# Optimization experiments

Measured on AMD Instinct MI355X. Metric: run time of the kernel, lower is better.

Reference implementation:

```python
import jax, jax.numpy as jnp
import numpy as np

ALPHA = 0.2  # LeakyReLU negative slope used by GAT attention


def _seg_softmax(scores, rows, n):
    # numerically stable softmax of per-edge scores grouped by destination row
    m = jax.ops.segment_max(scores, rows, num_segments=n)
    ex = jnp.exp(scores - m[rows])
    s = jax.ops.segment_sum(ex, rows, num_segments=n)
    return ex / s[rows]


def setup_inputs() -> dict:
    key = jax.random.key(0)
    ks = jax.random.split(key, 10)
    VOCAB, U, N, DEG = 200000, 50000, 20000, 16
    DIN, DOUT, H, ETYPES, EDIM = 64, 64, 4, 32, 64
    node_features = jax.random.normal(ks[0], (VOCAB, DIN), jnp.float32)
    W = jax.random.normal(ks[1], (H, DIN, DOUT), jnp.float32) * np.float32(np.sqrt(2.0 / (DIN + DOUT)))
    a_pos = jax.random.normal(ks[2], (H, 2 * DOUT), jnp.float32) * 0.1
    a_neg = jax.random.normal(ks[3], (H, 2 * DOUT), jnp.float32) * 0.1
    edge_embedding = jax.random.normal(ks[4], (ETYPES, EDIM), jnp.float32)
    edge_transform = jax.random.normal(ks[5], (EDIM, DOUT), jnp.float32) * np.float32(np.sqrt(2.0 / (EDIM + DOUT)))
    unique_nodes = jax.random.randint(ks[6], (U,), 0, VOCAB)
    row_unique = jax.random.randint(ks[7], (N,), 0, U)  # index of each output row's own node in the unique list
    # pos adjacency with self edges appended (adj_pos2 in the source)
    pos_row = jnp.concatenate([jnp.repeat(jnp.arange(N), DEG), jnp.arange(N)])
    pos_col = jnp.concatenate([jax.random.randint(ks[8], (N * DEG,), 0, U), row_unique])
    neg_row = jnp.repeat(jnp.arange(N), DEG)
    neg_col = jax.random.randint(ks[9], (N * DEG,), 0, U)
    return {
        "node_features": node_features, "W": W, "a_pos": a_pos, "a_neg": a_neg,
        "edge_embedding": edge_embedding, "edge_transform": edge_transform,
        "unique_nodes": unique_nodes, "row_unique": row_unique,
        "pos_row": pos_row, "pos_col": pos_col, "neg_row": neg_row, "neg_col": neg_col,
        "n_rows": N,
    }


def reference(node_features, W, a_pos, a_neg, edge_embedding, edge_transform,
              unique_nodes, row_unique, pos_row, pos_col, neg_row, neg_col, n_rows):
    embed = node_features[unique_nodes]                 # [U, Din] gather of unique node embeddings
    Wh = jnp.einsum('ud,hdo->huo', embed, W)            # [H, U, Dout]
    Dout = W.shape[-1]
    rows_all = jnp.concatenate([pos_row, neg_row])
    cols_all = jnp.concatenate([pos_col, neg_col])

    def head(Wh_h, ap, an):
        # per-node score halves (GAT trick: a^T[h_i || h_j] = a_dst.h_i + a_src.h_j)
        dst_p = (Wh_h @ ap[:Dout])[row_unique]          # [N]
        src_p = Wh_h @ ap[Dout:]                        # [U]
        dst_n = (Wh_h @ an[:Dout])[row_unique]
        src_n = Wh_h @ an[Dout:]
        e_pos = jax.nn.leaky_relu(dst_p[pos_row] + src_p[pos_col], ALPHA)
        e_neg = jax.nn.leaky_relu(dst_n[neg_row] + src_n[neg_col], ALPHA)
        att = _seg_softmax(jnp.concatenate([e_pos, e_neg]), rows_all, n_rows)  # joint softmax over pos+neg edges
        return jax.ops.segment_sum(att[:, None] * Wh_h[cols_all], rows_all, num_segments=n_rows)

    outs = jax.vmap(head)(Wh, a_pos, a_neg)             # [H, N, Dout]
    h_hidden = jax.nn.relu(jnp.transpose(outs, (1, 0, 2)).reshape(outs.shape[1], -1))  # concat heads -> ReLU
    edge_out = edge_embedding @ edge_transform          # edge-type projection
    return (h_hidden, edge_out)
```

## Files before the change

kernel.cpp:

```cpp
#include <hip/hip_runtime.h>
#include <hip/hip_bf16.h>
#include <hip/hip_fp16.h>
#include <math.h>

#define LRELU_ALPHA 0.2f

typedef __attribute__((ext_vector_type(8))) short bf16x8;
typedef __attribute__((ext_vector_type(4))) float f32x4;
typedef _Float16 f16x8 __attribute__((ext_vector_type(8)));

__device__ __forceinline__ unsigned short f2bf(float f) {
    union { float f; unsigned u; } v; v.f = f;
    unsigned r = v.u + 0x7fffu + ((v.u >> 16) & 1u);
    return (unsigned short)(r >> 16);
}
__device__ __forceinline__ unsigned short f2h(float f) {
    union { __half h; unsigned short s; } c; c.h = __float2half_rn(f); return c.s;
}
__device__ __forceinline__ unsigned cvtpk(float lo, float hi) {
    unsigned r;
    asm("v_cvt_pk_bf16_f32 %0, %1, %2" : "=v"(r) : "v"(lo), "v"(hi));
    return r;
}
__device__ __forceinline__ __half2 u2h2(unsigned u) {
    union { unsigned u; __half2 h; } x; x.u = u; return x.h;
}
__device__ __forceinline__ unsigned h22u(__half2 h) {
    union { __half2 h; unsigned u; } x; x.h = h; return x.u;
}
__device__ __forceinline__ float2 upk(unsigned u) {
    return __half22float2(u2h2(u));
}

__global__ void prep_kernel(const float* __restrict__ W,
                            const float* __restrict__ a_pos, const float* __restrict__ a_neg,
                            const float* __restrict__ ee, const float* __restrict__ et,
                            unsigned short* __restrict__ Wt, unsigned short* __restrict__ avB,
                            float* __restrict__ edge_out, int H, int ET) {
    const int HE = H * 4096, AV = H * 256;
    int t = blockIdx.x * blockDim.x + threadIdx.x;
    if (t < HE) {
        int k = t & 63, n = (t >> 6) & 63, h = t >> 12;
        Wt[((size_t)h * 64 + n) * 64 + k] = f2h(W[(size_t)h * 4096 + k * 64 + n]);
    } else if (t < HE + AV) {
        int s = t - HE;
        int k = s & 63, q = (s >> 6) & 3, h = s >> 8;
        const float* a  = (q < 2 ? a_pos : a_neg) + (size_t)h * 128 + (q & 1) * 64;
        const float* wr = W + (size_t)h * 4096 + k * 64;
        float v = 0.f;
#pragma unroll
        for (int o = 0; o < 64; o += 4) {
            const float4 wv = *(const float4*)(wr + o);
            const float4 av = *(const float4*)(a + o);
            v = fmaf(wv.x, av.x, fmaf(wv.y, av.y, fmaf(wv.z, av.z, fmaf(wv.w, av.w, v))));
        }
        avB[((size_t)h * 4 + q) * 64 + k] = f2bf(v);
    } else {
        int s = t - HE - AV;
        if (s < ET * 64) {
            int e = s >> 6, o = s & 63;
            float acc = 0.f;
#pragma unroll
            for (int k = 0; k < 64; ++k)
                acc = fmaf(ee[e * 64 + k], et[k * 64 + o], acc);
            edge_out[s] = acc;
        }
    }
}

__global__ __launch_bounds__(256) void score_cvt_kernel(
    const float* __restrict__ nf, const unsigned short* __restrict__ avB,
    const int* __restrict__ un, unsigned short* __restrict__ embed16,
    unsigned* __restrict__ scd, unsigned* __restrict__ scs, int U)
{
    const int wave = threadIdx.x >> 6;
    const int lane = threadIdx.x & 63;
    const int grp  = lane >> 4;
    const int r    = lane & 15;
    const long u0  = (long)blockIdx.x * 64 + wave * 16;
    if (u0 >= U) return;
    const long u  = u0 + r;
    const long ur = (u < U) ? u : (long)(U - 1);

    const float* erow = nf + (size_t)un[ur] * 64 + grp * 8;
    const float4 e0 = *(const float4*)(erow);
    const float4 e1 = *(const float4*)(erow + 4);
    const float4 e2 = *(const float4*)(erow + 32);
    const float4 e3 = *(const float4*)(erow + 36);

    union { unsigned d[4]; bf16x8 v; } A0, A1;
    A0.d[0] = cvtpk(e0.x, e0.y); A0.d[1] = cvtpk(e0.z, e0.w);
    A0.d[2] = cvtpk(e1.x, e1.y); A0.d[3] = cvtpk(e1.z, e1.w);
    A1.d[0] = cvtpk(e2.x, e2.y); A1.d[1] = cvtpk(e2.z, e2.w);
    A1.d[2] = cvtpk(e3.x, e3.y); A1.d[3] = cvtpk(e3.z, e3.w);

    if (u < U) {
        union { __half2 h2[4]; uint4 v; } F0, F1;
        F0.h2[0] = __floats2half2_rn(e0.x, e0.y); F0.h2[1] = __floats2half2_rn(e0.z, e0.w);
        F0.h2[2] = __floats2half2_rn(e1.x, e1.y); F0.h2[3] = __floats2half2_rn(e1.z, e1.w);
        F1.h2[0] = __floats2half2_rn(e2.x, e2.y); F1.h2[1] = __floats2half2_rn(e2.z, e2.w);
        F1.h2[2] = __floats2half2_rn(e3.x, e3.y); F1.h2[3] = __floats2half2_rn(e3.z, e3.w);
        *(uint4*)(embed16 + (size_t)u * 64 + grp * 8)      = F0.v;
        *(uint4*)(embed16 + (size_t)u * 64 + 32 + grp * 8) = F1.v;
    }

    f32x4 acc = (f32x4)(0.f);
    const unsigned short* wp = avB + (size_t)r * 64 + grp * 8;
    bf16x8 b0 = *(const bf16x8*)wp;
    bf16x8 b1 = *(const bf16x8*)(wp + 32);
    acc = __builtin_amdgcn_mfma_f32_16x16x32_bf16(b0, A0.v, acc, 0, 0, 0);
    acc = __builtin_amdgcn_mfma_f32_16x16x32_bf16(b1, A1.v, acc, 0, 0, 0);

    if (u < U) {
        scd[(size_t)u * 4 + grp] = h22u(__floats2half2_rn(acc[0], acc[2]));
        scs[(size_t)u * 4 + grp] = h22u(__floats2half2_rn(acc[1], acc[3]));
    }
}

__global__ __launch_bounds__(512) void aggemm_kernel(
    const int* __restrict__ pos_col, const int* __restrict__ neg_col,
    const unsigned short* __restrict__ embed16,
    const unsigned* __restrict__ scd, const unsigned* __restrict__ scs,
    const unsigned short* __restrict__ Wt,
    float* __restrict__ out, int N, int U)
{
    constexpr int DP = 16, NE = 33, NEP = 36;
    __shared__ int   s_col[8][2][NEP];
    __shared__ uint4 s_att[8][2][NEP];
    __shared__ __align__(16) unsigned short s_agg[16][256];

    const int wave = threadIdx.x >> 6;
    const int lane = threadIdx.x & 63;
    const int iA = blockIdx.x * 16 + wave * 2;
    const int iB = iA + 1;

    int colA = 0, colB = 0;
    if (lane < DP)       { colA = pos_col[(size_t)iA * DP + lane];
                           colB = pos_col[(size_t)iB * DP + lane]; }
    else if (lane == DP) { colA = pos_col[(size_t)N * DP + iA];
                           colB = pos_col[(size_t)N * DP + iB]; }
    else if (lane < NE)  { colA = neg_col[(size_t)iA * 16 + (lane - DP - 1)];
                           colB = neg_col[(size_t)iB * 16 + (lane - DP - 1)]; }

    const uint4 svA = *(const uint4*)(scs + (size_t)(unsigned)colA * 4);
    const uint4 svB = *(const uint4*)(scs + (size_t)(unsigned)colB * 4);
    const int uA = __shfl(colA, DP, 64), uB = __shfl(colB, DP, 64);
    const uint4 dvA = *(const uint4*)(scd + (size_t)(unsigned)uA * 4);
    const uint4 dvB = *(const uint4*)(scd + (size_t)(unsigned)uB * 4);

    const bool isp = (lane <= DP);
    float2 sA_0 = upk(svA.x), sA_1 = upk(svA.y), sA_2 = upk(svA.z), sA_3 = upk(svA.w);
    float2 sB_0 = upk(svB.x), sB_1 = upk(svB.y), sB_2 = upk(svB.z), sB_3 = upk(svB.w);
    float2 dA_0 = upk(dvA.x), dA_1 = upk(dvA.y), dA_2 = upk(dvA.z), dA_3 = upk(dvA.w);
    float2 dB_0 = upk(dvB.x), dB_1 = upk(dvB.y), dB_2 = upk(dvB.z), dB_3 = upk(dvB.w);
    float a_s0 = isp ? dA_0.x + sA_0.x : dA_0.y + sA_0.y;
    float a_s1 = isp ? dA_1.x + sA_1.x : dA_1.y + sA_1.y;
    float a_s2 = isp ? dA_2.x + sA_2.x : dA_2.y + sA_2.y;
    float a_s3 = isp ? dA_3.x + sA_3.x : dA_3.y + sA_3.y;
    float b_s0 = isp ? dB_0.x + sB_0.x : dB_0.y + sB_0.y;
    float b_s1 = isp ? dB_1.x + sB_1.x : dB_1.y + sB_1.y;
    float b_s2 = isp ? dB_2.x + sB_2.x : dB_2.y + sB_2.y;
    float b_s3 = isp ? dB_3.x + sB_3.x : dB_3.y + sB_3.y;
    a_s0 = (a_s0 > 0.f) ? a_s0 : LRELU_ALPHA * a_s0;
    a_s1 = (a_s1 > 0.f) ? a_s1 : LRELU_ALPHA * a_s1;
    a_s2 = (a_s2 > 0.f) ? a_s2 : LRELU_ALPHA * a_s2;
    a_s3 = (a_s3 > 0.f) ? a_s3 : LRELU_ALPHA * a_s3;
    b_s0 = (b_s0 > 0.f) ? b_s0 : LRELU_ALPHA * b_s0;
    b_s1 = (b_s1 > 0.f) ? b_s1 : LRELU_ALPHA * b_s1;
    b_s2 = (b_s2 > 0.f) ? b_s2 : LRELU_ALPHA * b_s2;
    b_s3 = (b_s3 > 0.f) ? b_s3 : LRELU_ALPHA * b_s3;

    const bool act = (lane < NE);
    float ax0 = act ? __expf(a_s0) : 0.f, ax1 = act ? __expf(a_s1) : 0.f;
    float ax2 = act ? __expf(a_s2) : 0.f, ax3 = act ? __expf(a_s3) : 0.f;
    float bx0 = act ? __expf(b_s0) : 0.f, bx1 = act ? __expf(b_s1) : 0.f;
    float bx2 = act ? __expf(b_s2) : 0.f, bx3 = act ? __expf(b_s3) : 0.f;
    float aS0 = ax0, aS1 = ax1, aS2 = ax2, aS3 = ax3;
    float bS0 = bx0, bS1 = bx1, bS2 = bx2, bS3 = bx3;
#pragma unroll
    for (int off = 32; off; off >>= 1) {
        aS0 += __shfl_xor(aS0, off, 64); aS1 += __shfl_xor(aS1, off, 64);
        aS2 += __shfl_xor(aS2, off, 64); aS3 += __shfl_xor(aS3, off, 64);
        bS0 += __shfl_xor(bS0, off, 64); bS1 += __shfl_xor(bS1, off, 64);
        bS2 += __shfl_xor(bS2, off, 64); bS3 += __shfl_xor(bS3, off, 64);
    }
    if (lane < NEP) {
        uint4 tA, tB;
        tA.x = h22u(__float2half2_rn(__fdividef(ax0, aS0)));
        tA.y = h22u(__float2half2_rn(__fdividef(ax1, aS1)));
        tA.z = h22u(__float2half2_rn(__fdividef(ax2, aS2)));
        tA.w = h22u(__float2half2_rn(__fdividef(ax3, aS3)));
        tB.x = h22u(__float2half2_rn(__fdividef(bx0, bS0)));
        tB.y = h22u(__float2half2_rn(__fdividef(bx1, bS1)));
        tB.z = h22u(__float2half2_rn(__fdividef(bx2, bS2)));
        tB.w = h22u(__float2half2_rn(__fdividef(bx3, bS3)));
        s_col[wave][0][lane] = colA;  s_att[wave][0][lane] = tA;
        s_col[wave][1][lane] = colB;  s_att[wave][1][lane] = tB;
    }

    const int sub = lane >> 4;
    const int c   = lane & 15;
    const char* eb = (const char*)embed16 + (c << 3);
    __half2 accA[4][2], accB[4][2];
#pragma unroll
    for (int h = 0; h < 4; ++h)
#pragma unroll
        for (int d = 0; d < 2; ++d) {
            accA[h][d] = __float2half2_rn(0.f);
            accB[h][d] = __float2half2_rn(0.f);
        }
#pragma unroll
    for (int t = 0; t < 9; ++t) {
        const int   e  = 4 * t + sub;
        const int   cA = s_col[wave][0][e];
        const int   cB = s_col[wave][1][e];
        const uint2 vA = *(const uint2*)(eb + ((size_t)(unsigned)cA << 7));
        const uint2 vB = *(const uint2*)(eb + ((size_t)(unsigned)cB << 7));
        const uint4 tA = s_att[wave][0][e];
        const uint4 tB = s_att[wave][1][e];
        const __half2 vA0 = u2h2(vA.x), vA1 = u2h2(vA.y);
        const __half2 vB0 = u2h2(vB.x), vB1 = u2h2(vB.y);
        accA[0][0] = __hfma2(u2h2(tA.x), vA0, accA[0][0]);
        accA[0][1] = __hfma2(u2h2(tA.x), vA1, accA[0][1]);
        accA[1][0] = __hfma2(u2h2(tA.y), vA0, accA[1][0]);
        accA[1][1] = __hfma2(u2h2(tA.y), vA1, accA[1][1]);
        accA[2][0] = __hfma2(u2h2(tA.z), vA0, accA[2][0]);
        accA[2][1] = __hfma2(u2h2(tA.z), vA1, accA[2][1]);
        accA[3][0] = __hfma2(u2h2(tA.w), vA0, accA[3][0]);
        accA[3][1] = __hfma2(u2h2(tA.w), vA1, accA[3][1]);
        accB[0][0] = __hfma2(u2h2(tB.x), vB0, accB[0][0]);
        accB[0][1] = __hfma2(u2h2(tB.x), vB1, accB[0][1]);
        accB[1][0] = __hfma2(u2h2(tB.y), vB0, accB[1][0]);
        accB[1][1] = __hfma2(u2h2(tB.y), vB1, accB[1][1]);
        accB[2][0] = __hfma2(u2h2(tB.z), vB0, accB[2][0]);
        accB[2][1] = __hfma2(u2h2(tB.z), vB1, accB[2][1]);
        accB[3][0] = __hfma2(u2h2(tB.w), vB0, accB[3][0]);
        accB[3][1] = __hfma2(u2h2(tB.w), vB1, accB[3][1]);
    }
#pragma unroll
    for (int h = 0; h < 4; ++h)
#pragma unroll
        for (int d = 0; d < 2; ++d) {
            unsigned ua = h22u(accA[h][d]);
            ua = h22u(__hadd2(u2h2(ua), u2h2((unsigned)__shfl_xor((int)ua, 16, 64))));
            ua = h22u(__hadd2(u2h2(ua), u2h2((unsigned)__shfl_xor((int)ua, 32, 64))));
            accA[h][d] = u2h2(ua);
            unsigned ub = h22u(accB[h][d]);
            ub = h22u(__hadd2(u2h2(ub), u2h2((unsigned)__shfl_xor((int)ub, 16, 64))));
            ub = h22u(__hadd2(u2h2(ub), u2h2((unsigned)__shfl_xor((int)ub, 32, 64))));
            accB[h][d] = u2h2(ub);
        }
    if (sub == 0) {
#pragma unroll
        for (int h = 0; h < 4; ++h) {
            uint2 wA, wB;
            wA.x = h22u(accA[h][0]); wA.y = h22u(accA[h][1]);
            wB.x = h22u(accB[h][0]); wB.y = h22u(accB[h][1]);
            *(uint2*)((char*)&s_agg[wave * 2][h * 64] + c * 8)     = wA;
            *(uint2*)((char*)&s_agg[wave * 2 + 1][h * 64] + c * 8) = wB;
        }
    }
    __syncthreads();

    if (wave < 4) {
        const int h   = wave;
        const int grp = lane >> 4;
        const int r   = lane & 15;
        const f16x8 a0 = *(const f16x8*)((const char*)&s_agg[r][h * 64] + grp * 16);
        const f16x8 a1 = *(const f16x8*)((const char*)&s_agg[r][h * 64 + 32] + grp * 16);
        f32x4 acc[4];
#pragma unroll
        for (int nt = 0; nt < 4; ++nt) {
            acc[nt] = (f32x4)(0.f);
            const unsigned short* wp = Wt + (((size_t)h * 64 + nt * 16 + r) * 64 + grp * 8);
            const f16x8 b0 = *(const f16x8*)wp;
            const f16x8 b1 = *(const f16x8*)(wp + 32);
            acc[nt] = __builtin_amdgcn_mfma_f32_16x16x32_f16(b0, a0, acc[nt], 0, 0, 0);
            acc[nt] = __builtin_amdgcn_mfma_f32_16x16x32_f16(b1, a1, acc[nt], 0, 0, 0);
        }
        float* orow = out + ((size_t)(blockIdx.x * 16 + r) * 4 + h) * 64;
#pragma unroll
        for (int nt = 0; nt < 4; ++nt) {
            float4 o;
            o.x = fmaxf(acc[nt][0], 0.f); o.y = fmaxf(acc[nt][1], 0.f);
            o.z = fmaxf(acc[nt][2], 0.f); o.w = fmaxf(acc[nt][3], 0.f);
            *(float4*)(orow + nt * 16 + grp * 4) = o;
        }
    }
}

__global__ void embed_cvt_generic(const float* __restrict__ nf, const int* __restrict__ un,
                                  unsigned short* __restrict__ embed16, int U) {
    long t = (long)blockIdx.x * blockDim.x + threadIdx.x;
    if (t >= (long)U * 64) return;
    embed16[t] = f2h(nf[(size_t)un[t >> 6] * 64 + (t & 63)]);
}
__global__ void score_generic(const unsigned short* __restrict__ embed16,
                              const unsigned short* __restrict__ avB,
                              unsigned* __restrict__ scd, unsigned* __restrict__ scs,
                              int U, int H) {
    long t = (long)blockIdx.x * blockDim.x + threadIdx.x;
    if (t >= (long)U * H) return;
    const long u = t / H; const int h = (int)(t % H);
    float s[4];
    for (int q = 0; q < 4; ++q) {
        float acc = 0.f;
        for (int k = 0; k < 64; ++k) {
            union { unsigned short s; __half h; } w; w.s = embed16[u * 64 + k];
            union { unsigned uu; float f; } b;
            b.uu = ((unsigned)avB[((size_t)h * 4 + q) * 64 + k]) << 16;
            acc = fmaf(__half2float(w.h), b.f, acc);
        }
        s[q] = acc;
    }
    scd[u * H + h] = h22u(__floats2half2_rn(s[0], s[2]));
    scs[u * H + h] = h22u(__floats2half2_rn(s[1], s[3]));
}
__global__ __launch_bounds__(256) void agg_generic(
    const int* __restrict__ pos_col, const int* __restrict__ neg_col,
    const unsigned short* __restrict__ embed16,
    const unsigned* __restrict__ scd, const unsigned* __restrict__ scs,
    unsigned short* __restrict__ aggb, int N, int U, int DEGP, int DEGN, int H)
{
    const int wave = threadIdx.x >> 6;
    const int lane = threadIdx.x & 63;
    const long j = (long)blockIdx.x * 4 + wave;
    const int i = (int)(j % N);
    const int h = (int)(j / N);
    if (h >= H) return;
    const int NE = DEGP + 1 + DEGN;

    int col = 0;
    if (lane < DEGP)       col = pos_col[(size_t)i * DEGP + lane];
    else if (lane == DEGP) col = pos_col[(size_t)N * DEGP + i];
    else if (lane < NE)    col = neg_col[(size_t)i * DEGN + (lane - DEGP - 1)];
    const float2 ss = upk(scs[(size_t)col * H + h]);
    const int u0s = __shfl(col, DEGP, 64);
    const float2 sd = upk(scd[(size_t)u0s * H + h]);
    float score = -INFINITY;
    if (lane < NE) {
        const float raw = (lane <= DEGP) ? sd.x + ss.x : sd.y + ss.y;
        score = (raw > 0.f) ? raw : LRELU_ALPHA * raw;
    }
    float m = score;
#pragma unroll
    for (int off = 32; off; off >>= 1) m = fmaxf(m, __shfl_xor(m, off, 64));
    const float ex = (lane < NE) ? __expf(score - m) : 0.f;
    float S = ex;
#pragma unroll
    for (int off = 32; off; off >>= 1) S += __shfl_xor(S, off, 64);
    const float att = __fdividef(ex, S);

    float acc = 0.f;
    for (int e = 0; e < NE; ++e) {
        const int   ce = __shfl(col, e, 64);
        const float ae = __shfl(att, e, 64);
        union { unsigned short s; __half h; } w;
        w.s = embed16[(size_t)(unsigned)ce * 64 + lane];
        acc = fmaf(ae, __half2float(w.h), acc);
    }
    aggb[((size_t)i * H + h) * 64 + lane] = f2h(acc);
}
__global__ __launch_bounds__(256) void out_gemm_generic(
    const unsigned short* __restrict__ aggb, const unsigned short* __restrict__ Wt,
    float* __restrict__ out, int N, int H)
{
    const int wave = threadIdx.x >> 6;
    const int lane = threadIdx.x & 63;
    const int grp  = lane >> 4;
    const int r    = lane & 15;
    const long j = (long)blockIdx.x * 4 + wave;
    const int  h = (int)(j % H);
    const long i0 = (j / H) * 16;
    if (i0 >= N) return;
    const long i  = i0 + r;
    const long ir = (i < N) ? i : (long)(N - 1);

    const unsigned short* arow = aggb + ((size_t)ir * H + h) * 64 + grp * 8;
    const f16x8 a0 = *(const f16x8*)arow;
    const f16x8 a1 = *(const f16x8*)(arow + 32);
    f32x4 acc[4];
#pragma unroll
    for (int nt = 0; nt < 4; ++nt) {
        acc[nt] = (f32x4)(0.f);
        const unsigned short* wp = Wt + (((size_t)h * 64 + nt * 16 + r) * 64 + grp * 8);
        const f16x8 b0 = *(const f16x8*)wp;
        const f16x8 b1 = *(const f16x8*)(wp + 32);
        acc[nt] = __builtin_amdgcn_mfma_f32_16x16x32_f16(b0, a0, acc[nt], 0, 0, 0);
        acc[nt] = __builtin_amdgcn_mfma_f32_16x16x32_f16(b1, a1, acc[nt], 0, 0, 0);
    }
    if (i < N) {
        float* orow = out + ((size_t)i * H + h) * 64;
#pragma unroll
        for (int nt = 0; nt < 4; ++nt) {
            float4 o;
            o.x = fmaxf(acc[nt][0], 0.f); o.y = fmaxf(acc[nt][1], 0.f);
            o.z = fmaxf(acc[nt][2], 0.f); o.w = fmaxf(acc[nt][3], 0.f);
            *(float4*)(orow + nt * 16 + grp * 4) = o;
        }
    }
}

extern "C" void kernel_launch(void* const* d_in, const int* in_sizes, int n_in,
                              void* d_out, int out_size, void* d_ws, size_t ws_size,
                              hipStream_t stream) {
    const float* nf     = (const float*)d_in[0];
    const float* W      = (const float*)d_in[1];
    const float* a_pos  = (const float*)d_in[2];
    const float* a_neg  = (const float*)d_in[3];
    const float* ee     = (const float*)d_in[4];
    const float* et     = (const float*)d_in[5];
    const int* unique_nodes = (const int*)d_in[6];
    const int* pos_col  = (const int*)d_in[9];
    const int* neg_col  = (const int*)d_in[11];

    const int U    = in_sizes[6];
    const int N    = in_sizes[7];
    const int Epos = in_sizes[8];
    const int Eneg = in_sizes[10];
    const int H    = in_sizes[1] / (64 * 64);
    const int DEGN = Eneg / N;
    const int DEGP = Epos / N - 1;
    const int ET   = in_sizes[4] / 64;

    char* ws = (char*)d_ws;
    auto alloc = [&](size_t bytes) { char* p = ws; ws += (bytes + 255) & ~(size_t)255; return p; };
    unsigned short* embed16 = (unsigned short*)alloc((size_t)U * 64 * 2);
    unsigned*       scd     = (unsigned*)alloc((size_t)U * H * 4);
    unsigned*       scs     = (unsigned*)alloc((size_t)U * H * 4);
    unsigned short* aggb    = (unsigned short*)alloc((size_t)N * H * 64 * 2);
    unsigned short* Wt      = (unsigned short*)alloc((size_t)H * 4096 * 2);
    unsigned short* avB     = (unsigned short*)alloc((size_t)H * 256 * 2);
    float* out = (float*)d_out;

    const int PT = H * 4096 + H * 256 + ET * 64;
    prep_kernel<<<(PT + 255) / 256, 256, 0, stream>>>(W, a_pos, a_neg, ee, et, Wt, avB,
                                                      out + (size_t)N * H * 64, H, ET);

    if (H == 4 && DEGP == 16 && DEGN == 16 && (N % 16) == 0) {
        score_cvt_kernel<<<(U + 63) / 64, 256, 0, stream>>>(nf, avB, unique_nodes,
                                                            embed16, scd, scs, U);
        aggemm_kernel<<<N / 16, 512, 0, stream>>>(pos_col, neg_col, embed16,
                                                  scd, scs, Wt, out, N, U);
    } else {
        embed_cvt_generic<<<(int)(((long)U * 64 + 255) / 256), 256, 0, stream>>>(
            nf, unique_nodes, embed16, U);
        score_generic<<<(int)(((long)U * H + 255) / 256), 256, 0, stream>>>(
            embed16, avB, scd, scs, U, H);
        agg_generic<<<(int)(((long)N * H + 3) / 4), 256, 0, stream>>>(
            pos_col, neg_col, embed16, scd, scs, aggb, N, U, DEGP, DEGN, H);
        const long tiles = ((long)N + 15) / 16;
        out_gemm_generic<<<(int)((tiles * H + 3) / 4), 256, 0, stream>>>(aggb, Wt, out, N, H);
    }
}
```

Baseline: 45.60 us.

## Process four rows per wave in aggregation and move W transpose into score kernel

The aggregation kernel now handles 32 rows per block (four per wave instead of two), so all eight waves run the MFMA output GEMM rather than only four. The Wt transpose/convert moves out of prep_kernel into extra blocks of score_cvt_kernel, which shrinks the prep kernel. The aim is more memory-level parallelism per wave and fuller use of the waves in the GEMM phase. In exchange, register pressure and shared memory per block rise, and the block count halves, which can reduce occupancy.

```diff
diff --git a/kernel.cpp b/kernel.cpp
--- a/kernel.cpp
+++ b/kernel.cpp
@@ -35,16 +35,12 @@
 __global__ void prep_kernel(const float* __restrict__ W,
                             const float* __restrict__ a_pos, const float* __restrict__ a_neg,
                             const float* __restrict__ ee, const float* __restrict__ et,
-                            unsigned short* __restrict__ Wt, unsigned short* __restrict__ avB,
-                            float* __restrict__ edge_out, int H, int ET) {
-    const int HE = H * 4096, AV = H * 256;
+                            unsigned short* __restrict__ avB, float* __restrict__ edge_out,
+                            int H, int ET) {
+    const int AV = H * 256;
     int t = blockIdx.x * blockDim.x + threadIdx.x;
-    if (t < HE) {
-        int k = t & 63, n = (t >> 6) & 63, h = t >> 12;
-        Wt[((size_t)h * 64 + n) * 64 + k] = f2h(W[(size_t)h * 4096 + k * 64 + n]);
-    } else if (t < HE + AV) {
-        int s = t - HE;
-        int k = s & 63, q = (s >> 6) & 3, h = s >> 8;
+    if (t < AV) {
+        int k = t & 63, q = (t >> 6) & 3, h = t >> 8;
         const float* a  = (q < 2 ? a_pos : a_neg) + (size_t)h * 128 + (q & 1) * 64;
         const float* wr = W + (size_t)h * 4096 + k * 64;
         float v = 0.f;
@@ -56,7 +52,7 @@
         }
         avB[((size_t)h * 4 + q) * 64 + k] = f2bf(v);
     } else {
-        int s = t - HE - AV;
+        int s = t - AV;
         if (s < ET * 64) {
             int e = s >> 6, o = s & 63;
             float acc = 0.f;
@@ -70,9 +66,18 @@
 
 __global__ __launch_bounds__(256) void score_cvt_kernel(
     const float* __restrict__ nf, const unsigned short* __restrict__ avB,
-    const int* __restrict__ un, unsigned short* __restrict__ embed16,
-    unsigned* __restrict__ scd, unsigned* __restrict__ scs, int U)
+    const int* __restrict__ un, const float* __restrict__ W,
+    unsigned short* __restrict__ embed16, unsigned short* __restrict__ Wt,
+    unsigned* __restrict__ scd, unsigned* __restrict__ scs, int U, int UB, int H)
 {
+    if ((int)blockIdx.x >= UB) {
+        int t = (blockIdx.x - UB) * 256 + threadIdx.x;
+        if (t < H * 4096) {
+            int k = t & 63, n = (t >> 6) & 63, h = t >> 12;
+            Wt[((size_t)h * 64 + n) * 64 + k] = f2h(W[(size_t)h * 4096 + k * 64 + n]);
+        }
+        return;
+    }
     const int wave = threadIdx.x >> 6;
     const int lane = threadIdx.x & 63;
     const int grp  = lane >> 4;
@@ -125,170 +130,146 @@
     float* __restrict__ out, int N, int U)
 {
     constexpr int DP = 16, NE = 33, NEP = 36;
-    __shared__ int   s_col[8][2][NEP];
-    __shared__ uint4 s_att[8][2][NEP];
-    __shared__ __align__(16) unsigned short s_agg[16][256];
+    __shared__ int   s_col[8][4][NEP];
+    __shared__ uint4 s_att[8][4][NEP];
+    __shared__ __align__(16) unsigned short s_agg[32][256];
 
     const int wave = threadIdx.x >> 6;
     const int lane = threadIdx.x & 63;
-    const int iA = blockIdx.x * 16 + wave * 2;
-    const int iB = iA + 1;
-
-    int colA = 0, colB = 0;
-    if (lane < DP)       { colA = pos_col[(size_t)iA * DP + lane];
-                           colB = pos_col[(size_t)iB * DP + lane]; }
-    else if (lane == DP) { colA = pos_col[(size_t)N * DP + iA];
-                           colB = pos_col[(size_t)N * DP + iB]; }
-    else if (lane < NE)  { colA = neg_col[(size_t)iA * 16 + (lane - DP - 1)];
-                           colB = neg_col[(size_t)iB * 16 + (lane - DP - 1)]; }
-
-    const uint4 svA = *(const uint4*)(scs + (size_t)(unsigned)colA * 4);
-    const uint4 svB = *(const uint4*)(scs + (size_t)(unsigned)colB * 4);
-    const int uA = __shfl(colA, DP, 64), uB = __shfl(colB, DP, 64);
-    const uint4 dvA = *(const uint4*)(scd + (size_t)(unsigned)uA * 4);
-    const uint4 dvB = *(const uint4*)(scd + (size_t)(unsigned)uB * 4);
-
-    const bool isp = (lane <= DP);
-    float2 sA_0 = upk(svA.x), sA_1 = upk(svA.y), sA_2 = upk(svA.z), sA_3 = upk(svA.w);
-    float2 sB_0 = upk(svB.x), sB_1 = upk(svB.y), sB_2 = upk(svB.z), sB_3 = upk(svB.w);
-    float2 dA_0 = upk(dvA.x), dA_1 = upk(dvA.y), dA_2 = upk(dvA.z), dA_3 = upk(dvA.w);
-    float2 dB_0 = upk(dvB.x), dB_1 = upk(dvB.y), dB_2 = upk(dvB.z), dB_3 = upk(dvB.w);
-    float a_s0 = isp ? dA_0.x + sA_0.x : dA_0.y + sA_0.y;
-    float a_s1 = isp ? dA_1.x + sA_1.x : dA_1.y + sA_1.y;
-    float a_s2 = isp ? dA_2.x + sA_2.x : dA_2.y + sA_2.y;
-    float a_s3 = isp ? dA_3.x + sA_3.x : dA_3.y + sA_3.y;
-    float b_s0 = isp ? dB_0.x + sB_0.x : dB_0.y + sB_0.y;
-    float b_s1 = isp ? dB_1.x + sB_1.x : dB_1.y + sB_1.y;
-    float b_s2 = isp ? dB_2.x + sB_2.x : dB_2.y + sB_2.y;
-    float b_s3 = isp ? dB_3.x + sB_3.x : dB_3.y + sB_3.y;
-    a_s0 = (a_s0 > 0.f) ? a_s0 : LRELU_ALPHA * a_s0;
-    a_s1 = (a_s1 > 0.f) ? a_s1 : LRELU_ALPHA * a_s1;
-    a_s2 = (a_s2 > 0.f) ? a_s2 : LRELU_ALPHA * a_s2;
-    a_s3 = (a_s3 > 0.f) ? a_s3 : LRELU_ALPHA * a_s3;
-    b_s0 = (b_s0 > 0.f) ? b_s0 : LRELU_ALPHA * b_s0;
-    b_s1 = (b_s1 > 0.f) ? b_s1 : LRELU_ALPHA * b_s1;
-    b_s2 = (b_s2 > 0.f) ? b_s2 : LRELU_ALPHA * b_s2;
-    b_s3 = (b_s3 > 0.f) ? b_s3 : LRELU_ALPHA * b_s3;
-
-    const bool act = (lane < NE);
-    float ax0 = act ? __expf(a_s0) : 0.f, ax1 = act ? __expf(a_s1) : 0.f;
-    float ax2 = act ? __expf(a_s2) : 0.f, ax3 = act ? __expf(a_s3) : 0.f;
-    float bx0 = act ? __expf(b_s0) : 0.f, bx1 = act ? __expf(b_s1) : 0.f;
-    float bx2 = act ? __expf(b_s2) : 0.f, bx3 = act ? __expf(b_s3) : 0.f;
-    float aS0 = ax0, aS1 = ax1, aS2 = ax2, aS3 = ax3;
-    float bS0 = bx0, bS1 = bx1, bS2 = bx2, bS3 = bx3;
-#pragma unroll
-    for (int off = 32; off; off >>= 1) {
-        aS0 += __shfl_xor(aS0, off, 64); aS1 += __shfl_xor(aS1, off, 64);
-        aS2 += __shfl_xor(aS2, off, 64); aS3 += __shfl_xor(aS3, off, 64);
-        bS0 += __shfl_xor(bS0, off, 64); bS1 += __shfl_xor(bS1, off, 64);
-        bS2 += __shfl_xor(bS2, off, 64); bS3 += __shfl_xor(bS3, off, 64);
-    }
-    if (lane < NEP) {
-        uint4 tA, tB;
-        tA.x = h22u(__float2half2_rn(__fdividef(ax0, aS0)));
-        tA.y = h22u(__float2half2_rn(__fdividef(ax1, aS1)));
-        tA.z = h22u(__float2half2_rn(__fdividef(ax2, aS2)));
-        tA.w = h22u(__float2half2_rn(__fdividef(ax3, aS3)));
-        tB.x = h22u(__float2half2_rn(__fdividef(bx0, bS0)));
-        tB.y = h22u(__float2half2_rn(__fdividef(bx1, bS1)));
-        tB.z = h22u(__float2half2_rn(__fdividef(bx2, bS2)));
-        tB.w = h22u(__float2half2_rn(__fdividef(bx3, bS3)));
-        s_col[wave][0][lane] = colA;  s_att[wave][0][lane] = tA;
-        s_col[wave][1][lane] = colB;  s_att[wave][1][lane] = tB;
+    const int ibase = blockIdx.x * 32 + wave * 4;
+
+#pragma unroll
+    for (int rr = 0; rr < 4; ++rr) {
+        const int i = ibase + rr;
+        int col = 0;
+        if (lane < DP)       col = pos_col[(size_t)i * DP + lane];
+        else if (lane == DP) col = pos_col[(size_t)N * DP + i];
+        else if (lane < NE)  col = neg_col[(size_t)i * 16 + (lane - DP - 1)];
+
+        const uint4 sv = *(const uint4*)(scs + (size_t)(unsigned)col * 4);
+        const int uD = __shfl(col, DP, 64);
+        const uint4 dv = *(const uint4*)(scd + (size_t)(unsigned)uD * 4);
+
+        const bool isp = (lane <= DP);
+        float2 s_0 = upk(sv.x), s_1 = upk(sv.y), s_2 = upk(sv.z), s_3 = upk(sv.w);
+        float2 d_0 = upk(dv.x), d_1 = upk(dv.y), d_2 = upk(dv.z), d_3 = upk(dv.w);
+        float c0 = isp ? d_0.x + s_0.x : d_0.y + s_0.y;
+        float c1 = isp ? d_1.x + s_1.x : d_1.y + s_1.y;
+        float c2 = isp ? d_2.x + s_2.x : d_2.y + s_2.y;
+        float c3 = isp ? d_3.x + s_3.x : d_3.y + s_3.y;
+        c0 = (c0 > 0.f) ? c0 : LRELU_ALPHA * c0;
+        c1 = (c1 > 0.f) ? c1 : LRELU_ALPHA * c1;
+        c2 = (c2 > 0.f) ? c2 : LRELU_ALPHA * c2;
+        c3 = (c3 > 0.f) ? c3 : LRELU_ALPHA * c3;
+
+        const bool act = (lane < NE);
+        float x0 = act ? __expf(c0) : 0.f, x1 = act ? __expf(c1) : 0.f;
+        float x2 = act ? __expf(c2) : 0.f, x3 = act ? __expf(c3) : 0.f;
+        float S0 = x0, S1 = x1, S2 = x2, S3 = x3;
+#pragma unroll
+        for (int off = 32; off; off >>= 1) {
+            S0 += __shfl_xor(S0, off, 64); S1 += __shfl_xor(S1, off, 64);
+            S2 += __shfl_xor(S2, off, 64); S3 += __shfl_xor(S3, off, 64);
+        }
+        if (lane < NEP) {
+            uint4 t4;
+            t4.x = h22u(__float2half2_rn(__fdividef(x0, S0)));
+            t4.y = h22u(__float2half2_rn(__fdividef(x1, S1)));
+            t4.z = h22u(__float2half2_rn(__fdividef(x2, S2)));
+            t4.w = h22u(__float2half2_rn(__fdividef(x3, S3)));
+            s_col[wave][rr][lane] = col;
+            s_att[wave][rr][lane] = t4;
+        }
     }
 
     const int sub = lane >> 4;
     const int c   = lane & 15;
     const char* eb = (const char*)embed16 + (c << 3);
-    __half2 accA[4][2], accB[4][2];
-#pragma unroll
-    for (int h = 0; h < 4; ++h)
-#pragma unroll
-        for (int d = 0; d < 2; ++d) {
-            accA[h][d] = __float2half2_rn(0.f);
-            accB[h][d] = __float2half2_rn(0.f);
-        }
+    __half2 acc[4][4][2];
+#pragma unroll
+    for (int rr = 0; rr < 4; ++rr)
+#pragma unroll
+        for (int h = 0; h < 4; ++h)
+#pragma unroll
+            for (int d = 0; d < 2; ++d)
+                acc[rr][h][d] = __float2half2_rn(0.f);
 #pragma unroll
     for (int t = 0; t < 9; ++t) {
-        const int   e  = 4 * t + sub;
-        const int   cA = s_col[wave][0][e];
-        const int   cB = s_col[wave][1][e];
-        const uint2 vA = *(const uint2*)(eb + ((size_t)(unsigned)cA << 7));
-        const uint2 vB = *(const uint2*)(eb + ((size_t)(unsigned)cB << 7));
-        const uint4 tA = s_att[wave][0][e];
-        const uint4 tB = s_att[wave][1][e];
-        const __half2 vA0 = u2h2(vA.x), vA1 = u2h2(vA.y);
-        const __half2 vB0 = u2h2(vB.x), vB1 = u2h2(vB.y);
-        accA[0][0] = __hfma2(u2h2(tA.x), vA0, accA[0][0]);
-        accA[0][1] = __hfma2(u2h2(tA.x), vA1, accA[0][1]);
-        accA[1][0] = __hfma2(u2h2(tA.y), vA0, accA[1][0]);
-        accA[1][1] = __hfma2(u2h2(tA.y), vA1, accA[1][1]);
-        accA[2][0] = __hfma2(u2h2(tA.z), vA0, accA[2][0]);
-        accA[2][1] = __hfma2(u2h2(tA.z), vA1, accA[2][1]);
-        accA[3][0] = __hfma2(u2h2(tA.w), vA0, accA[3][0]);
-        accA[3][1] = __hfma2(u2h2(tA.w), vA1, accA[3][1]);
-        accB[0][0] = __hfma2(u2h2(tB.x), vB0, accB[0][0]);
-        accB[0][1] = __hfma2(u2h2(tB.x), vB1, accB[0][1]);
-        accB[1][0] = __hfma2(u2h2(tB.y), vB0, accB[1][0]);
-        accB[1][1] = __hfma2(u2h2(tB.y), vB1, accB[1][1]);
-        accB[2][0] = __hfma2(u2h2(tB.z), vB0, accB[2][0]);
-        accB[2][1] = __hfma2(u2h2(tB.z), vB1, accB[2][1]);
-        accB[3][0] = __hfma2(u2h2(tB.w), vB0, accB[3][0]);
-        accB[3][1] = __hfma2(u2h2(tB.w), vB1, accB[3][1]);
-    }
-#pragma unroll
-    for (int h = 0; h < 4; ++h)
-#pragma unroll
-        for (int d = 0; d < 2; ++d) {
-            unsigned ua = h22u(accA[h][d]);
-            ua = h22u(__hadd2(u2h2(ua), u2h2((unsigned)__shfl_xor((int)ua, 16, 64))));
-            ua = h22u(__hadd2(u2h2(ua), u2h2((unsigned)__shfl_xor((int)ua, 32, 64))));
-            accA[h][d] = u2h2(ua);
-            unsigned ub = h22u(accB[h][d]);
-            ub = h22u(__hadd2(u2h2(ub), u2h2((unsigned)__shfl_xor((int)ub, 16, 64))));
-            ub = h22u(__hadd2(u2h2(ub), u2h2((unsigned)__shfl_xor((int)ub, 32, 64))));
-            accB[h][d] = u2h2(ub);
-        }
+        const int e = 4 * t + sub;
+#pragma unroll
+        for (int rr = 0; rr < 4; ++rr) {
+            const int   cc = s_col[wave][rr][e];
+            const uint2 vv = *(const uint2*)(eb + ((size_t)(unsigned)cc << 7));
+            const uint4 t4 = s_att[wave][rr][e];
+            const __half2 v0 = u2h2(vv.x), v1 = u2h2(vv.y);
+            acc[rr][0][0] = __hfma2(u2h2(t4.x), v0, acc[rr][0][0]);
+            acc[rr][0][1] = __hfma2(u2h2(t4.x), v1, acc[rr][0][1]);
+            acc[rr][1][0] = __hfma2(u2h2(t4.y), v0, acc[rr][1][0]);
+            acc[rr][1][1] = __hfma2(u2h2(t4.y), v1, acc[rr][1][1]);
+            acc[rr][2][0] = __hfma2(u2h2(t4.z), v0, acc[rr][2][0]);
+            acc[rr][2][1] = __hfma2(u2h2(t4.z), v1, acc[rr][2][1]);
+            acc[rr][3][0] = __hfma2(u2h2(t4.w), v0, acc[rr][3][0]);
+            acc[rr][3][1] = __hfma2(u2h2(t4.w), v1, acc[rr][3][1]);
+        }
+    }
+#pragma unroll
+    for (int rr = 0; rr < 4; ++rr)
+#pragma unroll
+        for (int h = 0; h < 4; ++h)
+#pragma unroll
+            for (int d = 0; d < 2; ++d) {
+                unsigned ua = h22u(acc[rr][h][d]);
+                ua = h22u(__hadd2(u2h2(ua), u2h2((unsigned)__shfl_xor((int)ua, 16, 64))));
+                ua = h22u(__hadd2(u2h2(ua), u2h2((unsigned)__shfl_xor((int)ua, 32, 64))));
+                acc[rr][h][d] = u2h2(ua);
+            }
     if (sub == 0) {
 #pragma unroll
-        for (int h = 0; h < 4; ++h) {
-            uint2 wA, wB;
-            wA.x = h22u(accA[h][0]); wA.y = h22u(accA[h][1]);
-            wB.x = h22u(accB[h][0]); wB.y = h22u(accB[h][1]);
-            *(uint2*)((char*)&s_agg[wave * 2][h * 64] + c * 8)     = wA;
-            *(uint2*)((char*)&s_agg[wave * 2 + 1][h * 64] + c * 8) = wB;
-        }
+        for (int rr = 0; rr < 4; ++rr)
+#pragma unroll
+            for (int h = 0; h < 4; ++h) {
+                uint2 w2;
+                w2.x = h22u(acc[rr][h][0]); w2.y = h22u(acc[rr][h][1]);
+                *(uint2*)((char*)&s_agg[wave * 4 + rr][h * 64] + c * 8) = w2;
+            }
     }
     __syncthreads();
 
-    if (wave < 4) {
-        const int h   = wave;
+    {
+        const int h   = wave & 3;
+        const int rb  = wave >> 2;
         const int grp = lane >> 4;
         const int r   = lane & 15;
-        const f16x8 a0 = *(const f16x8*)((const char*)&s_agg[r][h * 64] + grp * 16);
-        const f16x8 a1 = *(const f16x8*)((const char*)&s_agg[r][h * 64 + 32] + grp * 16);
-        f32x4 acc[4];
+        const int row = rb * 16 + r;
+        const f16x8 a0 = *(const f16x8*)((const char*)&s_agg[row][h * 64] + grp * 16);
+        const f16x8 a1 = *(const f16x8*)((const char*)&s_agg[row][h * 64 + 32] + grp * 16);
+        f32x4 acc2[4];
 #pragma unroll
         for (int nt = 0; nt < 4; ++nt) {
-            acc[nt] = (f32x4)(0.f);
+            acc2[nt] = (f32x4)(0.f);
             const unsigned short* wp = Wt + (((size_t)h * 64 + nt * 16 + r) * 64 + grp * 8);
             const f16x8 b0 = *(const f16x8*)wp;
             const f16x8 b1 = *(const f16x8*)(wp + 32);
-            acc[nt] = __builtin_amdgcn_mfma_f32_16x16x32_f16(b0, a0, acc[nt], 0, 0, 0);
-            acc[nt] = __builtin_amdgcn_mfma_f32_16x16x32_f16(b1, a1, acc[nt], 0, 0, 0);
-        }
-        float* orow = out + ((size_t)(blockIdx.x * 16 + r) * 4 + h) * 64;
+            acc2[nt] = __builtin_amdgcn_mfma_f32_16x16x32_f16(b0, a0, acc2[nt], 0, 0, 0);
+            acc2[nt] = __builtin_amdgcn_mfma_f32_16x16x32_f16(b1, a1, acc2[nt], 0, 0, 0);
+        }
+        float* orow = out + ((size_t)(blockIdx.x * 32 + row) * 4 + h) * 64;
 #pragma unroll
         for (int nt = 0; nt < 4; ++nt) {
             float4 o;
-            o.x = fmaxf(acc[nt][0], 0.f); o.y = fmaxf(acc[nt][1], 0.f);
-            o.z = fmaxf(acc[nt][2], 0.f); o.w = fmaxf(acc[nt][3], 0.f);
+            o.x = fmaxf(acc2[nt][0], 0.f); o.y = fmaxf(acc2[nt][1], 0.f);
+            o.z = fmaxf(acc2[nt][2], 0.f); o.w = fmaxf(acc2[nt][3], 0.f);
             *(float4*)(orow + nt * 16 + grp * 4) = o;
         }
     }
 }
 
+__global__ void wt_generic(const float* __restrict__ W, unsigned short* __restrict__ Wt, int HE) {
+    int t = blockIdx.x * blockDim.x + threadIdx.x;
+    if (t >= HE) return;
+    int k = t & 63, n = (t >> 6) & 63, h = t >> 12;
+    Wt[((size_t)h * 64 + n) * 64 + k] = f2h(W[(size_t)h * 4096 + k * 64 + n]);
+}
 __global__ void embed_cvt_generic(const float* __restrict__ nf, const int* __restrict__ un,
                                   unsigned short* __restrict__ embed16, int U) {
     long t = (long)blockIdx.x * blockDim.x + threadIdx.x;
@@ -433,16 +414,19 @@
     unsigned short* avB     = (unsigned short*)alloc((size_t)H * 256 * 2);
     float* out = (float*)d_out;
 
-    const int PT = H * 4096 + H * 256 + ET * 64;
-    prep_kernel<<<(PT + 255) / 256, 256, 0, stream>>>(W, a_pos, a_neg, ee, et, Wt, avB,
+    const int PT = H * 256 + ET * 64;
+    prep_kernel<<<(PT + 255) / 256, 256, 0, stream>>>(W, a_pos, a_neg, ee, et, avB,
                                                       out + (size_t)N * H * 64, H, ET);
 
-    if (H == 4 && DEGP == 16 && DEGN == 16 && (N % 16) == 0) {
-        score_cvt_kernel<<<(U + 63) / 64, 256, 0, stream>>>(nf, avB, unique_nodes,
-                                                            embed16, scd, scs, U);
-        aggemm_kernel<<<N / 16, 512, 0, stream>>>(pos_col, neg_col, embed16,
+    if (H == 4 && DEGP == 16 && DEGN == 16 && (N % 32) == 0) {
+        const int UB = (U + 63) / 64;
+        const int WTB = (H * 4096 + 255) / 256;
+        score_cvt_kernel<<<UB + WTB, 256, 0, stream>>>(nf, avB, unique_nodes, W,
+                                                       embed16, Wt, scd, scs, U, UB, H);
+        aggemm_kernel<<<N / 32, 512, 0, stream>>>(pos_col, neg_col, embed16,
                                                   scd, scs, Wt, out, N, U);
     } else {
+        wt_generic<<<(H * 4096 + 255) / 256, 256, 0, stream>>>(W, Wt, H * 4096);
         embed_cvt_generic<<<(int)(((long)U * 64 + 255) / 256), 256, 0, stream>>>(
             nf, unique_nodes, embed16, U);
         score_generic<<<(int)(((long)U * H + 255) / 256), 256, 0, stream>>>(
```

After: 52.52 us. 1.15x slower.
